# Performance work log

Hardware: AMD Instinct MI355X
Metric: run time of the kernel (lower is better)

The kernel has to match this reference:

```python
import jax, jax.numpy as jnp
import numpy as np

N = 100000          # total nodes
E = 1600000         # edges
C = 128             # in_channels
H = 256             # hidden_size
ACT_DIM = 20        # nodes per graph -> batch = N // ACT_DIM


def setup_inputs() -> dict:
    key = jax.random.key(0)
    ks = jax.random.split(key, 10)
    x = jax.random.normal(ks[0], (N, C), dtype=jnp.float32)
    edge_index = jax.random.randint(ks[1], (2, E), 0, N, dtype=jnp.int64)
    s = 0.05
    conv_w = jax.random.normal(ks[2], (C, C), dtype=jnp.float32) * s   # [in, out]
    conv_b = jnp.zeros((C,), dtype=jnp.float32)
    lin1_w = jax.random.normal(ks[3], (H, C), dtype=jnp.float32) * s   # torch [out, in]
    lin1_b = jnp.zeros((H,), dtype=jnp.float32)
    lin2_w = jax.random.normal(ks[4], (H, H), dtype=jnp.float32) * s
    lin2_b = jnp.zeros((H,), dtype=jnp.float32)
    lin3_w = jax.random.normal(ks[5], (1, H), dtype=jnp.float32) * s
    lin3_b = jnp.zeros((1,), dtype=jnp.float32)
    return {"x": x, "edge_index": edge_index,
            "conv_w": conv_w, "conv_b": conv_b,
            "lin1_w": lin1_w, "lin1_b": lin1_b,
            "lin2_w": lin2_w, "lin2_b": lin2_b,
            "lin3_w": lin3_w, "lin3_b": lin3_b}


def gcn_conv(x, edge_index, w, b):
    """PyG GCNConv: x' = D^{-1/2} (A + I) D^{-1/2} (x W) + b."""
    n = x.shape[0]
    loops = jnp.arange(n, dtype=edge_index.dtype)
    src = jnp.concatenate([edge_index[0], loops])  # [E + N]
    dst = jnp.concatenate([edge_index[1], loops])
    deg = jax.ops.segment_sum(jnp.ones_like(dst, dtype=x.dtype), dst, num_segments=n)
    dinv = jnp.where(deg > 0, jax.lax.rsqrt(deg), 0.0)
    norm = dinv[src] * dinv[dst]                   # [E + N]
    xw = x @ w                                     # [N, out]
    msg = xw[src] * norm[:, None]                  # gather + scale, [E+N, out]
    out = jax.ops.segment_sum(msg, dst, num_segments=n)  # scatter-add
    return out + b


def reference(x, edge_index, conv_w, conv_b, lin1_w, lin1_b, lin2_w, lin2_b, lin3_w, lin3_b):
    out = jax.nn.relu(gcn_conv(x, edge_index, conv_w, conv_b))
    h = out + x                                    # residual, [N, C]
    h = h.reshape(-1, ACT_DIM, C)                  # [B, act_dim, C]
    h = jax.nn.relu(h @ lin1_w.T + lin1_b)         # [B, act_dim, H]
    h = jax.nn.relu(h @ lin2_w.T + lin2_b)
    h = jnp.sum(h, axis=1)                         # [B, H]
    h = h @ lin3_w.T + lin3_b                      # [B, 1]
    if h.shape[0] == 1:                            # torch .squeeze(0) semantics
        h = h[0]
    return h
```

## Files before the change

kernel.cpp:

```cpp
#include <hip/hip_runtime.h>
#include <hip/hip_bf16.h>
#include <cstddef>

#define NNODES 100000
#define NEDGES 1600000
#define CIN 128
#define HID 256
#define ACT 20
#define NGRAPH (NNODES / ACT)
#define BSHIFT 8
#define NB ((NNODES + 255) >> 8)
#define BIN_WGS 512
#define PER_WG (NEDGES / BIN_WGS)
#define CAP 8192

typedef __attribute__((ext_vector_type(8))) short short8;
typedef __attribute__((ext_vector_type(4))) float f32x4;

__device__ __forceinline__ unsigned short f2b(float f) {
    unsigned u = __float_as_uint(f);
    u += 0x7FFF + ((u >> 16) & 1);
    return (unsigned short)(u >> 16);
}
__device__ __forceinline__ float b2f(unsigned short h) {
    return __uint_as_float(((unsigned)h) << 16);
}


__global__ __launch_bounds__(256) void bin_k(const int* __restrict__ ei,
                                             int* __restrict__ bfill,
                                             unsigned* __restrict__ entries) {
    __shared__ int cnt[NB], lofs[NB], base[NB], cur[NB];
    __shared__ unsigned lbuf[PER_WG];
    __shared__ int gdst[PER_WG];
    __shared__ int wsum[4];
    const int t = threadIdx.x;
    for (int i = t; i < NB; i += 256) { cnt[i] = 0; cur[i] = 0; }
    __syncthreads();
    const int s = blockIdx.x * PER_WG;
    const int e = s + PER_WG;
    for (int i = s + t; i < e; i += 256)
        atomicAdd(&cnt[ei[NEDGES + i] >> BSHIFT], 1);
    __syncthreads();
    int c0 = (2 * t < NB) ? cnt[2 * t] : 0;
    int c1 = (2 * t + 1 < NB) ? cnt[2 * t + 1] : 0;
    int v = c0 + c1;
    int lane = t & 63, wid = t >> 6;
    int inc = v;
#pragma unroll
    for (int o = 1; o < 64; o <<= 1) {
        int tv = __shfl_up(inc, o, 64);
        if (lane >= o) inc += tv;
    }
    if (lane == 63) wsum[wid] = inc;
    __syncthreads();
    int woff = 0;
#pragma unroll
    for (int w = 0; w < 4; ++w) woff += (w < wid) ? wsum[w] : 0;
    int excl = inc + woff - v;
    if (2 * t < NB) lofs[2 * t] = excl;
    if (2 * t + 1 < NB) lofs[2 * t + 1] = excl + c0;
    __syncthreads();
    for (int b = t; b < NB; b += 256)
        base[b] = cnt[b] ? atomicAdd(&bfill[b], cnt[b]) : 0;
    __syncthreads();
    for (int i = s + t; i < e; i += 256) {
        int src = ei[i], dst = ei[NEDGES + i];
        int b = dst >> BSHIFT;
        int r = atomicAdd(&cur[b], 1);
        int slot = lofs[b] + r;
        lbuf[slot] = ((unsigned)src << 8) | (unsigned)(dst & 255);
        int g = base[b] + r;
        gdst[slot] = (g < CAP) ? (int)((size_t)b * CAP + g) : -1;
    }
    __syncthreads();
    for (int i = t; i < PER_WG; i += 256) {
        int g = gdst[i];
        if (g >= 0) entries[g] = lbuf[i];
    }
}

__global__ __launch_bounds__(256) void bucket_build_k(
    const unsigned* __restrict__ entries, const int* __restrict__ bfill,
    int2* __restrict__ rowptr2, int* __restrict__ csr, float* __restrict__ dinv) {
    const int b = blockIdx.x;
    const int count = min(bfill[b], CAP);
    const int node0 = b << BSHIFT;
    const int nn = min(256, NNODES - node0);
    const size_t gbase = (size_t)b * CAP;
    __shared__ int cnt[256], off[256], cur[256];
    const int t = threadIdx.x;
    cnt[t] = 0; cur[t] = 0;
    __syncthreads();
    for (int i = t; i < count; i += 256)
        atomicAdd(&cnt[entries[gbase + i] & 255], 1);
    __syncthreads();
    int lane = t & 63, wid = t >> 6;
    int v = cnt[t];
    int inc = v;
#pragma unroll
    for (int o = 1; o < 64; o <<= 1) {
        int tv = __shfl_up(inc, o, 64);
        if (lane >= o) inc += tv;
    }
    __shared__ int wsum[4];
    if (lane == 63) wsum[wid] = inc;
    __syncthreads();
    int woff = 0;
#pragma unroll
    for (int w = 0; w < 4; ++w) woff += (w < wid) ? wsum[w] : 0;
    int excl = inc + woff - v;
    off[t] = excl;
    if (t < nn) {
        rowptr2[node0 + t] = make_int2((int)gbase + excl, (int)gbase + excl + v);
        dinv[node0 + t] = rsqrtf(1.0f + (float)v);
    }
    __syncthreads();
    for (int i = t; i < count; i += 256) {
        unsigned en = entries[gbase + i];
        int loc = (int)(en & 255);
        int r = atomicAdd(&cur[loc], 1);
        csr[gbase + off[loc] + r] = (int)(en >> 8);
    }
}


__global__ void cvt_w_k(const float* __restrict__ conv_w,
                        const float* __restrict__ lin1_w,
                        const float* __restrict__ lin2_w,
                        unsigned short* __restrict__ wt0,
                        unsigned short* __restrict__ wt1,
                        unsigned short* __restrict__ wt2) {
    int id = blockIdx.x * 256 + threadIdx.x;
    if (id < 16384) {
        int k = id >> 7, n = id & 127;
        wt0[n * 128 + k] = f2b(conv_w[k * 128 + n]);
    } else if (id < 16384 + 32768) {
        int i = id - 16384;
        wt1[i] = f2b(lin1_w[i]);
    } else if (id < 16384 + 32768 + 65536) {
        int i = id - 49152;
        wt2[i] = f2b(lin2_w[i]);
    }
}


__global__ __launch_bounds__(256) void mgemm0_k(
    const float* __restrict__ Af, const unsigned short* __restrict__ B,
    const float* __restrict__ dinv, unsigned short* __restrict__ Cout, int M)
{
    const int tid = threadIdx.x;
    const int wid = tid >> 6;
    const int lane = tid & 63;
    const int quad = lane >> 4;
    const int l16 = lane & 15;
    const int bm = blockIdx.x * 128 + (wid >> 1) * 64;
    const int bn = (wid & 1) * 64;

    const float* pa[4];
    const unsigned short* pb[4];
#pragma unroll
    for (int t = 0; t < 4; ++t) {
        int m = bm + t * 16 + l16; if (m >= M) m = M - 1;
        pa[t] = Af + (size_t)m * 128 + quad * 8;
        int n = bn + t * 16 + l16;
        pb[t] = B + (size_t)n * 128 + quad * 8;
    }

    f32x4 acc[4][4];
#pragma unroll
    for (int i = 0; i < 4; ++i)
#pragma unroll
        for (int j = 0; j < 4; ++j) {
            f32x4 z = {0.f, 0.f, 0.f, 0.f};
            acc[i][j] = z;
        }

    float4 afl[2][4][2];
    short8 bf[2][4];
#pragma unroll
    for (int t = 0; t < 4; ++t) {
        afl[0][t][0] = *reinterpret_cast<const float4*>(pa[t]);
        afl[0][t][1] = *reinterpret_cast<const float4*>(pa[t] + 4);
        bf[0][t] = *reinterpret_cast<const short8*>(pb[t]);
    }

#pragma unroll
    for (int kt = 0; kt < 4; ++kt) {
        const int cur = kt & 1, nxt = cur ^ 1;
        if (kt < 3) {
#pragma unroll
            for (int t = 0; t < 4; ++t) {
                afl[nxt][t][0] = *reinterpret_cast<const float4*>(pa[t] + (kt + 1) * 32);
                afl[nxt][t][1] = *reinterpret_cast<const float4*>(pa[t] + (kt + 1) * 32 + 4);
                bf[nxt][t] = *reinterpret_cast<const short8*>(pb[t] + (kt + 1) * 32);
            }
        }
        short8 a[4];
#pragma unroll
        for (int t = 0; t < 4; ++t) {
            float4 f0 = afl[cur][t][0], f1 = afl[cur][t][1];
            short8 av;
            av[0] = (short)f2b(f0.x); av[1] = (short)f2b(f0.y);
            av[2] = (short)f2b(f0.z); av[3] = (short)f2b(f0.w);
            av[4] = (short)f2b(f1.x); av[5] = (short)f2b(f1.y);
            av[6] = (short)f2b(f1.z); av[7] = (short)f2b(f1.w);
            a[t] = av;
        }
#pragma unroll
        for (int i = 0; i < 4; ++i)
#pragma unroll
            for (int j = 0; j < 4; ++j)
                acc[i][j] = __builtin_amdgcn_mfma_f32_16x16x32_bf16(a[i], bf[cur][j], acc[i][j], 0, 0, 0);
    }

#pragma unroll
    for (int i = 0; i < 4; ++i)
#pragma unroll
        for (int r = 0; r < 4; ++r) {
            int row = bm + i * 16 + quad * 4 + r;
            if (row >= M) continue;
            float dv = dinv[row];
#pragma unroll
            for (int j = 0; j < 4; ++j) {
                int col = bn + j * 16 + l16;
                Cout[(size_t)row * 128 + col] = f2b(acc[i][j][r] * dv);
            }
        }
}


__global__ __launch_bounds__(256) void gather_k(
    const int2* __restrict__ rowptr2, const int* __restrict__ csr,
    const unsigned short* __restrict__ xws, const float* __restrict__ dinv,
    const float* __restrict__ x, const float* __restrict__ conv_b,
    unsigned short* __restrict__ h0)
{
    const int node = blockIdx.x * 4 + (threadIdx.x >> 6);
    if (node >= NNODES) return;
    const int lane = threadIdx.x & 63;
    const int sub = lane >> 4;
    const int c16 = lane & 15;

    const int2 se = rowptr2[node];
    const int start = se.x, end = se.y;

    float2 s2[4];
    if (sub == 0) {
        uint4 v = *reinterpret_cast<const uint4*>(xws + (size_t)node * CIN + c16 * 8);
        unsigned d[4] = {v.x, v.y, v.z, v.w};
#pragma unroll
        for (int k = 0; k < 4; ++k) {
            s2[k].x = __uint_as_float(d[k] << 16);
            s2[k].y = __uint_as_float(d[k] & 0xffff0000u);
        }
    } else {
#pragma unroll
        for (int k = 0; k < 4; ++k) s2[k] = make_float2(0.f, 0.f);
    }

    for (int p = start; p < end; p += 32) {
        uint4 r[8];
        int valid[8];
#pragma unroll
        for (int j = 0; j < 8; ++j) {
            int e = p + j * 4 + sub;
            bool a = e < end;
            int idx = a ? csr[e] : node;
            r[j] = *reinterpret_cast<const uint4*>(xws + (size_t)idx * CIN + c16 * 8);
            valid[j] = a;
        }
#pragma unroll
        for (int j = 0; j < 8; ++j)
            if (valid[j]) {
                unsigned d[4] = {r[j].x, r[j].y, r[j].z, r[j].w};
#pragma unroll
                for (int k = 0; k < 4; ++k) {
                    s2[k].x += __uint_as_float(d[k] << 16);
                    s2[k].y += __uint_as_float(d[k] & 0xffff0000u);
                }
            }
    }

#pragma unroll
    for (int k = 0; k < 4; ++k) {
        s2[k].x += __shfl_xor(s2[k].x, 16, 64);
        s2[k].y += __shfl_xor(s2[k].y, 16, 64);
        s2[k].x += __shfl_xor(s2[k].x, 32, 64);
        s2[k].y += __shfl_xor(s2[k].y, 32, 64);
    }

    if (sub == 0) {
        float dvv = dinv[node];
        float4 b0 = *reinterpret_cast<const float4*>(conv_b + c16 * 8);
        float4 b1 = *reinterpret_cast<const float4*>(conv_b + c16 * 8 + 4);
        float4 x0 = *reinterpret_cast<const float4*>(x + (size_t)node * CIN + c16 * 8);
        float4 x1 = *reinterpret_cast<const float4*>(x + (size_t)node * CIN + c16 * 8 + 4);
        float o[8];
        o[0] = fmaxf(s2[0].x * dvv + b0.x, 0.f) + x0.x;
        o[1] = fmaxf(s2[0].y * dvv + b0.y, 0.f) + x0.y;
        o[2] = fmaxf(s2[1].x * dvv + b0.z, 0.f) + x0.z;
        o[3] = fmaxf(s2[1].y * dvv + b0.w, 0.f) + x0.w;
        o[4] = fmaxf(s2[2].x * dvv + b1.x, 0.f) + x1.x;
        o[5] = fmaxf(s2[2].y * dvv + b1.y, 0.f) + x1.y;
        o[6] = fmaxf(s2[3].x * dvv + b1.z, 0.f) + x1.z;
        o[7] = fmaxf(s2[3].y * dvv + b1.w, 0.f) + x1.w;
        short8 pk;
#pragma unroll
        for (int q = 0; q < 8; ++q) pk[q] = (short)f2b(o[q]);
        *reinterpret_cast<short8*>(h0 + (size_t)node * CIN + c16 * 8) = pk;
    }
}


__global__ __launch_bounds__(256) void fmlp_k(
    const unsigned short* __restrict__ h0, const unsigned short* __restrict__ w1,
    const float* __restrict__ b1, const unsigned short* __restrict__ w2,
    const float* __restrict__ b2, const float* __restrict__ w3,
    float* __restrict__ rowsum, int M)
{
    __shared__ unsigned short h1s[64 * 256];
    const int tid = threadIdx.x;
    const int wave = tid >> 6;
    const int lane = tid & 63;
    const int quad = lane >> 4;
    const int l16 = lane & 15;
    const int bm = blockIdx.x * 64;
    const int nc0 = wave * 64;

    f32x4 acc[4][4];
#pragma unroll
    for (int i = 0; i < 4; ++i)
#pragma unroll
        for (int j = 0; j < 4; ++j) {
            f32x4 z = {0.f, 0.f, 0.f, 0.f};
            acc[i][j] = z;
        }

    {
        const unsigned short* pa[4];
        const unsigned short* pb[4];
#pragma unroll
        for (int t = 0; t < 4; ++t) {
            int m = bm + t * 16 + l16; if (m >= M) m = M - 1;
            pa[t] = h0 + (size_t)m * 128 + quad * 8;
            int n = nc0 + t * 16 + l16;
            pb[t] = w1 + (size_t)n * 128 + quad * 8;
        }
        short8 af[2][4], bf[2][4];
#pragma unroll
        for (int t = 0; t < 4; ++t) {
            af[0][t] = *reinterpret_cast<const short8*>(pa[t]);
            bf[0][t] = *reinterpret_cast<const short8*>(pb[t]);
        }
#pragma unroll
        for (int kt = 0; kt < 4; ++kt) {
            const int cur = kt & 1, nxt = cur ^ 1;
            if (kt < 3) {
#pragma unroll
                for (int t = 0; t < 4; ++t) {
                    af[nxt][t] = *reinterpret_cast<const short8*>(pa[t] + (kt + 1) * 32);
                    bf[nxt][t] = *reinterpret_cast<const short8*>(pb[t] + (kt + 1) * 32);
                }
            }
#pragma unroll
            for (int i = 0; i < 4; ++i)
#pragma unroll
                for (int j = 0; j < 4; ++j)
                    acc[i][j] = __builtin_amdgcn_mfma_f32_16x16x32_bf16(af[cur][i], bf[cur][j], acc[i][j], 0, 0, 0);
        }
#pragma unroll
        for (int nt = 0; nt < 4; ++nt) {
            int col = nc0 + nt * 16 + l16;
            float bv = b1[col];
            int chunk = col >> 3, rem = col & 7;
#pragma unroll
            for (int mt = 0; mt < 4; ++mt)
#pragma unroll
                for (int r = 0; r < 4; ++r) {
                    int row = mt * 16 + quad * 4 + r;
                    h1s[row * 256 + (((chunk ^ (row & 7)) << 3) | rem)] =
                        f2b(fmaxf(acc[mt][nt][r] + bv, 0.f));
                }
        }
    }
    __syncthreads();

#pragma unroll
    for (int i = 0; i < 4; ++i)
#pragma unroll
        for (int j = 0; j < 4; ++j) {
            f32x4 z = {0.f, 0.f, 0.f, 0.f};
            acc[i][j] = z;
        }
    {
        const unsigned short* pb[4];
#pragma unroll
        for (int t = 0; t < 4; ++t) {
            int n = nc0 + t * 16 + l16;
            pb[t] = w2 + (size_t)n * 256 + quad * 8;
        }
        short8 af[3][4], bf[3][4];
#pragma unroll
        for (int t = 0; t < 4; ++t) {
            int row = t * 16 + l16;
            af[0][t] = *reinterpret_cast<const short8*>(
                &h1s[row * 256 + ((quad ^ (row & 7)) << 3)]);
            af[1][t] = *reinterpret_cast<const short8*>(
                &h1s[row * 256 + (((4 + quad) ^ (row & 7)) << 3)]);
            bf[0][t] = *reinterpret_cast<const short8*>(pb[t]);
            bf[1][t] = *reinterpret_cast<const short8*>(pb[t] + 32);
        }
#pragma unroll
        for (int kt = 0; kt < 8; ++kt) {
            const int cu = kt % 3, nx = (kt + 2) % 3;
            if (kt + 2 < 8) {
                const int c2 = (kt + 2) * 4 + quad;
#pragma unroll
                for (int t = 0; t < 4; ++t) {
                    int row = t * 16 + l16;
                    af[nx][t] = *reinterpret_cast<const short8*>(
                        &h1s[row * 256 + ((c2 ^ (row & 7)) << 3)]);
                    bf[nx][t] = *reinterpret_cast<const short8*>(pb[t] + (kt + 2) * 32);
                }
            }
#pragma unroll
            for (int i = 0; i < 4; ++i)
#pragma unroll
                for (int j = 0; j < 4; ++j)
                    acc[i][j] = __builtin_amdgcn_mfma_f32_16x16x32_bf16(af[cu][i], bf[cu][j], acc[i][j], 0, 0, 0);
        }
    }

    float part[4][4];
#pragma unroll
    for (int mt = 0; mt < 4; ++mt)
#pragma unroll
        for (int r = 0; r < 4; ++r) part[mt][r] = 0.f;
#pragma unroll
    for (int nt = 0; nt < 4; ++nt) {
        int col = nc0 + nt * 16 + l16;
        float bs = b2[col];
        float wv3 = w3[col];
#pragma unroll
        for (int mt = 0; mt < 4; ++mt)
#pragma unroll
            for (int r = 0; r < 4; ++r)
                part[mt][r] += fmaxf(acc[mt][nt][r] + bs, 0.f) * wv3;
    }
#pragma unroll
    for (int mt = 0; mt < 4; ++mt)
#pragma unroll
        for (int r = 0; r < 4; ++r) {
            float v = part[mt][r];
            v += __shfl_xor(v, 1, 64);
            v += __shfl_xor(v, 2, 64);
            v += __shfl_xor(v, 4, 64);
            v += __shfl_xor(v, 8, 64);
            part[mt][r] = v;
        }
    if (l16 == 0) {
#pragma unroll
        for (int mt = 0; mt < 4; ++mt)
#pragma unroll
            for (int r = 0; r < 4; ++r) {
                int row = bm + mt * 16 + quad * 4 + r;
                if (row < M) rowsum[(size_t)row * 4 + wave] = part[mt][r];
            }
    }
}


__global__ __launch_bounds__(256) void final_k(
    const float* __restrict__ rowsum, const float* __restrict__ b3,
    float* __restrict__ out)
{
    int g = blockIdx.x * 256 + threadIdx.x;
    if (g >= NGRAPH) return;
    const float4* p = reinterpret_cast<const float4*>(rowsum + (size_t)g * 80);
    float s = 0.f;
#pragma unroll
    for (int i = 0; i < 20; ++i) {
        float4 v = p[i];
        s += (v.x + v.y) + (v.z + v.w);
    }
    out[g] = s + b3[0];
}


extern "C" void kernel_launch(void* const* d_in, const int* in_sizes, int n_in,
                              void* d_out, int out_size, void* d_ws, size_t ws_size,
                              hipStream_t stream)
{
    const float* x      = (const float*)d_in[0];
    const int*   ei     = (const int*)  d_in[1];
    const float* conv_w = (const float*)d_in[2];
    const float* conv_b = (const float*)d_in[3];
    const float* lin1_w = (const float*)d_in[4];
    const float* lin1_b = (const float*)d_in[5];
    const float* lin2_w = (const float*)d_in[6];
    const float* lin2_b = (const float*)d_in[7];
    const float* lin3_w = (const float*)d_in[8];
    const float* lin3_b = (const float*)d_in[9];
    float* out = (float*)d_out;

    unsigned short* xws     = (unsigned short*)d_ws;
    unsigned short* h0      = xws + (size_t)12800000;
    unsigned*       entries = (unsigned*)(h0 + (size_t)12800000);
    int*            csr     = (int*)(entries + (size_t)NB * CAP);
    int2*           rowptr2 = (int2*)(csr + (size_t)NB * CAP);
    float*          dinv    = (float*)(rowptr2 + NNODES);
    int*            bfill   = (int*)(dinv + NNODES);
    unsigned short* wt0     = (unsigned short*)(bfill + NB + 8);
    unsigned short* wt1     = wt0 + 16384;
    unsigned short* wt2     = wt1 + 32768;
    float*          rowsum  = (float*)(wt2 + 65536);

    hipMemsetAsync(bfill, 0, NB * sizeof(int), stream);
    bin_k<<<BIN_WGS, 256, 0, stream>>>(ei, bfill, entries);
    bucket_build_k<<<NB, 256, 0, stream>>>(entries, bfill, rowptr2, csr, dinv);

    cvt_w_k<<<(114688 + 255) / 256, 256, 0, stream>>>(conv_w, lin1_w, lin2_w, wt0, wt1, wt2);

    mgemm0_k<<<(NNODES + 127) / 128, 256, 0, stream>>>(x, wt0, dinv, xws, NNODES);

    gather_k<<<(NNODES + 3) / 4, 256, 0, stream>>>(rowptr2, csr, xws, dinv, x, conv_b, h0);

    fmlp_k<<<(NNODES + 63) / 64, 256, 0, stream>>>(h0, wt1, lin1_b, wt2, lin2_b, lin3_w,
                                                   rowsum, NNODES);

    final_k<<<(NGRAPH + 255) / 256, 256, 0, stream>>>(rowsum, lin3_b, out);
}
```

Baseline: 301.6 us.

## Slice xW into channel planes for cache-local gather; move residual add into MLP

The GEMM output xW is now written as 8 planes of 16 channels each. The gather kernel runs 8 channel slices per node group, so each slice's working set (about 3.2 MB) can fit in L2 and the random neighbour reads hit cache more often. The residual add of x moves from the gather epilogue into the MLP's A-operand load. The cost is more blocks, each reading the CSR indices once per slice (8x the index traffic), narrower 8-byte loads, and an extra bf16 rounding step on the residual.

After: 456.1 us. +51.2%, slower.

```diff
diff --git a/kernel.cpp b/kernel.cpp
--- a/kernel.cpp
+++ b/kernel.cpp
@@ -13,6 +13,8 @@
 #define BIN_WGS 512
 #define PER_WG (NEDGES / BIN_WGS)
 #define CAP 8192
+#define NSLICE 8
+#define PLANE ((size_t)NNODES * 16)
 
 typedef __attribute__((ext_vector_type(8))) short short8;
 typedef __attribute__((ext_vector_type(4))) float f32x4;
@@ -223,8 +225,8 @@
             float dv = dinv[row];
 #pragma unroll
             for (int j = 0; j < 4; ++j) {
-                int col = bn + j * 16 + l16;
-                Cout[(size_t)row * 128 + col] = f2b(acc[i][j][r] * dv);
+                size_t pbase = (size_t)((bn >> 4) + j) * PLANE;
+                Cout[pbase + (size_t)row * 16 + l16] = f2b(acc[i][j][r] * dv);
             }
         }
 }
@@ -233,88 +235,94 @@
 __global__ __launch_bounds__(256) void gather_k(
     const int2* __restrict__ rowptr2, const int* __restrict__ csr,
     const unsigned short* __restrict__ xws, const float* __restrict__ dinv,
-    const float* __restrict__ x, const float* __restrict__ conv_b,
-    unsigned short* __restrict__ h0)
+    const float* __restrict__ conv_b, unsigned short* __restrict__ h0)
 {
-    const int node = blockIdx.x * 4 + (threadIdx.x >> 6);
-    if (node >= NNODES) return;
+    const int slice = blockIdx.x & 7;
+    const int ng = blockIdx.x >> 3;
+    const int wave = threadIdx.x >> 6;
     const int lane = threadIdx.x & 63;
-    const int sub = lane >> 4;
-    const int c16 = lane & 15;
-
-    const int2 se = rowptr2[node];
-    const int start = se.x, end = se.y;
-
-    float2 s2[4];
-    if (sub == 0) {
-        uint4 v = *reinterpret_cast<const uint4*>(xws + (size_t)node * CIN + c16 * 8);
-        unsigned d[4] = {v.x, v.y, v.z, v.w};
-#pragma unroll
-        for (int k = 0; k < 4; ++k) {
-            s2[k].x = __uint_as_float(d[k] << 16);
-            s2[k].y = __uint_as_float(d[k] & 0xffff0000u);
-        }
-    } else {
-#pragma unroll
-        for (int k = 0; k < 4; ++k) s2[k] = make_float2(0.f, 0.f);
-    }
-
-    for (int p = start; p < end; p += 32) {
-        uint4 r[8];
-        int valid[8];
-#pragma unroll
-        for (int j = 0; j < 8; ++j) {
-            int e = p + j * 4 + sub;
-            bool a = e < end;
-            int idx = a ? csr[e] : node;
-            r[j] = *reinterpret_cast<const uint4*>(xws + (size_t)idx * CIN + c16 * 8);
-            valid[j] = a;
-        }
-#pragma unroll
-        for (int j = 0; j < 8; ++j)
-            if (valid[j]) {
-                unsigned d[4] = {r[j].x, r[j].y, r[j].z, r[j].w};
-#pragma unroll
-                for (int k = 0; k < 4; ++k) {
-                    s2[k].x += __uint_as_float(d[k] << 16);
-                    s2[k].y += __uint_as_float(d[k] & 0xffff0000u);
+    const int eslot = lane >> 2;
+    const int cq = lane & 3;
+    const unsigned short* xp = xws + (size_t)slice * PLANE;
+
+#pragma unroll 1
+    for (int ni = 0; ni < 8; ++ni) {
+        const int node = ng * 32 + wave * 8 + ni;
+        const int2 se = rowptr2[node];
+        const int start = se.x, end = se.y;
+
+        float a0 = 0.f, a1 = 0.f, a2 = 0.f, a3 = 0.f;
+        if (eslot == 0) {
+            uint2 v = *reinterpret_cast<const uint2*>(xp + (size_t)node * 16 + cq * 4);
+            a0 = __uint_as_float(v.x << 16);
+            a1 = __uint_as_float(v.x & 0xffff0000u);
+            a2 = __uint_as_float(v.y << 16);
+            a3 = __uint_as_float(v.y & 0xffff0000u);
+        }
+
+        for (int p = start; p < end; p += 32) {
+            uint2 r[2];
+            int valid[2];
+#pragma unroll
+            for (int j = 0; j < 2; ++j) {
+                int e = p + j * 16 + eslot;
+                bool ok = e < end;
+                int idx = ok ? csr[e] : node;
+                r[j] = *reinterpret_cast<const uint2*>(xp + (size_t)idx * 16 + cq * 4);
+                valid[j] = ok;
+            }
+#pragma unroll
+            for (int j = 0; j < 2; ++j)
+                if (valid[j]) {
+                    a0 += __uint_as_float(r[j].x << 16);
+                    a1 += __uint_as_float(r[j].x & 0xffff0000u);
+                    a2 += __uint_as_float(r[j].y << 16);
+                    a3 += __uint_as_float(r[j].y & 0xffff0000u);
                 }
-            }
-    }
-
-#pragma unroll
-    for (int k = 0; k < 4; ++k) {
-        s2[k].x += __shfl_xor(s2[k].x, 16, 64);
-        s2[k].y += __shfl_xor(s2[k].y, 16, 64);
-        s2[k].x += __shfl_xor(s2[k].x, 32, 64);
-        s2[k].y += __shfl_xor(s2[k].y, 32, 64);
-    }
-
-    if (sub == 0) {
-        float dvv = dinv[node];
-        float4 b0 = *reinterpret_cast<const float4*>(conv_b + c16 * 8);
-        float4 b1 = *reinterpret_cast<const float4*>(conv_b + c16 * 8 + 4);
-        float4 x0 = *reinterpret_cast<const float4*>(x + (size_t)node * CIN + c16 * 8);
-        float4 x1 = *reinterpret_cast<const float4*>(x + (size_t)node * CIN + c16 * 8 + 4);
-        float o[8];
-        o[0] = fmaxf(s2[0].x * dvv + b0.x, 0.f) + x0.x;
-        o[1] = fmaxf(s2[0].y * dvv + b0.y, 0.f) + x0.y;
-        o[2] = fmaxf(s2[1].x * dvv + b0.z, 0.f) + x0.z;
-        o[3] = fmaxf(s2[1].y * dvv + b0.w, 0.f) + x0.w;
-        o[4] = fmaxf(s2[2].x * dvv + b1.x, 0.f) + x1.x;
-        o[5] = fmaxf(s2[2].y * dvv + b1.y, 0.f) + x1.y;
-        o[6] = fmaxf(s2[3].x * dvv + b1.z, 0.f) + x1.z;
-        o[7] = fmaxf(s2[3].y * dvv + b1.w, 0.f) + x1.w;
-        short8 pk;
-#pragma unroll
-        for (int q = 0; q < 8; ++q) pk[q] = (short)f2b(o[q]);
-        *reinterpret_cast<short8*>(h0 + (size_t)node * CIN + c16 * 8) = pk;
-    }
-}
-
+        }
+
+#pragma unroll
+        for (int m = 4; m < 64; m <<= 1) {
+            a0 += __shfl_xor(a0, m, 64);
+            a1 += __shfl_xor(a1, m, 64);
+            a2 += __shfl_xor(a2, m, 64);
+            a3 += __shfl_xor(a3, m, 64);
+        }
+
+        if (lane < 4) {
+            float dv = dinv[node];
+            float4 bv = *reinterpret_cast<const float4*>(conv_b + slice * 16 + lane * 4);
+            float o0 = fmaxf(a0 * dv + bv.x, 0.f);
+            float o1 = fmaxf(a1 * dv + bv.y, 0.f);
+            float o2 = fmaxf(a2 * dv + bv.z, 0.f);
+            float o3 = fmaxf(a3 * dv + bv.w, 0.f);
+            uint2 pk;
+            pk.x = (unsigned)f2b(o0) | ((unsigned)f2b(o1) << 16);
+            pk.y = (unsigned)f2b(o2) | ((unsigned)f2b(o3) << 16);
+            *reinterpret_cast<uint2*>(h0 + (size_t)node * CIN + slice * 16 + lane * 4) = pk;
+        }
+    }
+}
+
+
+__device__ __forceinline__ short8 addres(short8 h, const float* __restrict__ px) {
+    float4 f0 = *reinterpret_cast<const float4*>(px);
+    float4 f1 = *reinterpret_cast<const float4*>(px + 4);
+    short8 o;
+    o[0] = (short)f2b(b2f((unsigned short)h[0]) + f0.x);
+    o[1] = (short)f2b(b2f((unsigned short)h[1]) + f0.y);
+    o[2] = (short)f2b(b2f((unsigned short)h[2]) + f0.z);
+    o[3] = (short)f2b(b2f((unsigned short)h[3]) + f0.w);
+    o[4] = (short)f2b(b2f((unsigned short)h[4]) + f1.x);
+    o[5] = (short)f2b(b2f((unsigned short)h[5]) + f1.y);
+    o[6] = (short)f2b(b2f((unsigned short)h[6]) + f1.z);
+    o[7] = (short)f2b(b2f((unsigned short)h[7]) + f1.w);
+    return o;
+}
 
 __global__ __launch_bounds__(256) void fmlp_k(
-    const unsigned short* __restrict__ h0, const unsigned short* __restrict__ w1,
+    const unsigned short* __restrict__ h0, const float* __restrict__ xres,
+    const unsigned short* __restrict__ w1,
     const float* __restrict__ b1, const unsigned short* __restrict__ w2,
     const float* __restrict__ b2, const float* __restrict__ w3,
     float* __restrict__ rowsum, int M)
@@ -339,18 +347,20 @@
 
     {
         const unsigned short* pa[4];
+        const float* px[4];
         const unsigned short* pb[4];
 #pragma unroll
         for (int t = 0; t < 4; ++t) {
             int m = bm + t * 16 + l16; if (m >= M) m = M - 1;
             pa[t] = h0 + (size_t)m * 128 + quad * 8;
+            px[t] = xres + (size_t)m * 128 + quad * 8;
             int n = nc0 + t * 16 + l16;
             pb[t] = w1 + (size_t)n * 128 + quad * 8;
         }
         short8 af[2][4], bf[2][4];
 #pragma unroll
         for (int t = 0; t < 4; ++t) {
-            af[0][t] = *reinterpret_cast<const short8*>(pa[t]);
+            af[0][t] = addres(*reinterpret_cast<const short8*>(pa[t]), px[t]);
             bf[0][t] = *reinterpret_cast<const short8*>(pb[t]);
         }
 #pragma unroll
@@ -359,7 +369,8 @@
             if (kt < 3) {
 #pragma unroll
                 for (int t = 0; t < 4; ++t) {
-                    af[nxt][t] = *reinterpret_cast<const short8*>(pa[t] + (kt + 1) * 32);
+                    af[nxt][t] = addres(*reinterpret_cast<const short8*>(pa[t] + (kt + 1) * 32),
+                                        px[t] + (kt + 1) * 32);
                     bf[nxt][t] = *reinterpret_cast<const short8*>(pb[t] + (kt + 1) * 32);
                 }
             }
@@ -524,9 +535,9 @@
 
     mgemm0_k<<<(NNODES + 127) / 128, 256, 0, stream>>>(x, wt0, dinv, xws, NNODES);
 
-    gather_k<<<(NNODES + 3) / 4, 256, 0, stream>>>(rowptr2, csr, xws, dinv, x, conv_b, h0);
-
-    fmlp_k<<<(NNODES + 63) / 64, 256, 0, stream>>>(h0, wt1, lin1_b, wt2, lin2_b, lin3_w,
+    gather_k<<<(NNODES / 32) * NSLICE, 256, 0, stream>>>(rowptr2, csr, xws, dinv, conv_b, h0);
+
+    fmlp_k<<<(NNODES + 63) / 64, 256, 0, stream>>>(h0, x, wt1, lin1_b, wt2, lin2_b, lin3_w,
                                                    rowsum, NNODES);
 
     final_k<<<(NGRAPH + 255) / 256, 256, 0, stream>>>(rowsum, lin3_b, out);
```
